# Kernel optimization log

Measured on AMD Instinct MI355X. Metric: run time of the kernel, lower is better.

The kernel has to match this reference:

```python
import jax, jax.numpy as jnp
import numpy as np

N = 50000      # nodes
E_BASE = 400000  # random edges (avg degree 8)
E = E_BASE + N   # + self loops (added by add_self_loops in the torch code)
D = 128        # in_channels == hidden_output


def gcn_conv(x, src, dst, w, W, b, n_nodes):
    """PyG GCNConv with precomputed self-loops: h = x@W + b; symmetric-norm scatter-add."""
    h = x @ W + b                                            # [N, H]
    deg = jax.ops.segment_sum(w, dst, num_segments=n_nodes)  # weighted in-degree
    dinv = jnp.where(deg > 0, jax.lax.rsqrt(deg), 0.0)
    norm = dinv[src] * w * dinv[dst]                         # [E]
    msg = h[src] * norm[:, None]                             # gather + scale
    return jax.ops.segment_sum(msg, dst, num_segments=n_nodes)


def prelu(z, alpha):
    return jnp.where(z >= 0, z, alpha[None, :] * z)


def gconv(x, src, dst, w, W1, b1, W2, b2, alpha, n_nodes):
    z = prelu(gcn_conv(x, src, dst, w, W1, b1, n_nodes), alpha)
    z = prelu(gcn_conv(z, src, dst, w, W2, b2, n_nodes), alpha)
    return z


def setup_inputs() -> dict:
    key = jax.random.key(0)
    ks = jax.random.split(key, 12)
    src = jax.random.randint(ks[0], (E_BASE,), 0, N)
    dst = jax.random.randint(ks[1], (E_BASE,), 0, N)
    loops = jnp.arange(N, dtype=src.dtype)
    edge_index = jnp.stack([jnp.concatenate([src, loops]),
                            jnp.concatenate([dst, loops])])
    # |time_encoder| output used as edge weight -> positive; self-loop fill_value=1.0
    edge_weight = jnp.concatenate([
        jax.random.uniform(ks[2], (E_BASE,), minval=0.1, maxval=1.0),
        jnp.ones((N,), jnp.float32)])
    x = jax.random.normal(ks[3], (N, D), jnp.float32)
    s = 1.0 / np.sqrt(D)
    def lin(k):
        return jax.random.uniform(k, (D, D), jnp.float32, -s, s)
    return {
        "x": x, "edge_index": edge_index, "edge_weight": edge_weight,
        "perm1": jax.random.permutation(ks[4], N),
        "perm2": jax.random.permutation(ks[5], N),
        "W1a": lin(ks[6]), "b1a": jnp.zeros((D,), jnp.float32),
        "W2a": lin(ks[7]), "b2a": jnp.zeros((D,), jnp.float32),
        "alpha1": jnp.full((D,), 0.25, jnp.float32),
        "W1b": lin(ks[8]), "b1b": jnp.zeros((D,), jnp.float32),
        "W2b": lin(ks[9]), "b2b": jnp.zeros((D,), jnp.float32),
        "alpha2": jnp.full((D,), 0.25, jnp.float32),
        "projW": lin(ks[10]), "projb": jnp.zeros((D,), jnp.float32),
    }


def reference(x, edge_index, edge_weight, perm1, perm2,
              W1a, b1a, W2a, b2a, alpha1,
              W1b, b1b, W2b, b2b, alpha2, projW, projb):
    src, dst = edge_index[0], edge_index[1]
    n = x.shape[0]
    # two views (Identity augmentors), two encoders
    z1 = gconv(x, src, dst, edge_weight, W1a, b1a, W2a, b2a, alpha1, n)
    z2 = gconv(x, src, dst, edge_weight, W1b, b1b, W2b, b2b, alpha2, n)
    g1 = jax.nn.sigmoid(z1.mean(axis=0, keepdims=True)) @ projW + projb  # [1, H]
    g2 = jax.nn.sigmoid(z2.mean(axis=0, keepdims=True)) @ projW + projb
    # corruption: permute node features, keep graph structure
    z1n = gconv(x[perm1], src, dst, edge_weight, W1a, b1a, W2a, b2a, alpha1, n)
    z2n = gconv(x[perm2], src, dst, edge_weight, W1b, b1b, W2b, b2b, alpha2, n)
    return (z1, z2, g1, g2, z1n, z2n)
```

## Files before the change

kernel.cpp:

```cpp
#include <hip/hip_runtime.h>
#include <math.h>

#define D 128

typedef __attribute__((ext_vector_type(8))) short bf16x8;
typedef __attribute__((ext_vector_type(4))) float f32x4;

__device__ __forceinline__ unsigned short f2bf(float f) {
  unsigned u = __float_as_uint(f);
  unsigned r = (u + 0x7fffu + ((u >> 16) & 1u)) >> 16;
  return (unsigned short)r;
}
__device__ __forceinline__ unsigned pack2bf(float x, float y) {
  return (unsigned)f2bf(x) | ((unsigned)f2bf(y) << 16);
}
__device__ __forceinline__ float bf_lo(unsigned u) { return __uint_as_float(u << 16); }
__device__ __forceinline__ float bf_hi(unsigned u) { return __uint_as_float(u & 0xffff0000u); }


__global__ __launch_bounds__(256) void hist_k(const int* __restrict__ dst,
    const float* __restrict__ w, float* __restrict__ deg,
    int* __restrict__ cnt, int E) {
  int e = blockIdx.x * 256 + threadIdx.x;
  if (e < E) {
    int d = dst[e];
    atomicAdd(&deg[d], w[e]);
    atomicAdd(&cnt[d], 1);
  }
}

__global__ __launch_bounds__(256) void scan1_k(const int* __restrict__ cnt,
    int* __restrict__ offs, int* __restrict__ bsum, int n) {
  __shared__ int ls[256];
  int t = threadIdx.x;
  int base = blockIdx.x * 1024 + t * 4;
  int v0 = 0, v1 = 0, v2 = 0, v3 = 0;
  if (base + 0 < n) v0 = cnt[base + 0];
  if (base + 1 < n) v1 = cnt[base + 1];
  if (base + 2 < n) v2 = cnt[base + 2];
  if (base + 3 < n) v3 = cnt[base + 3];
  int s = v0 + v1 + v2 + v3;
  ls[t] = s;
  __syncthreads();
  for (int off = 1; off < 256; off <<= 1) {
    int x = 0;
    if (t >= off) x = ls[t - off];
    __syncthreads();
    if (t >= off) ls[t] += x;
    __syncthreads();
  }
  int run = (t > 0) ? ls[t - 1] : 0;
  if (base + 0 < n) offs[base + 0] = run; run += v0;
  if (base + 1 < n) offs[base + 1] = run; run += v1;
  if (base + 2 < n) offs[base + 2] = run; run += v2;
  if (base + 3 < n) offs[base + 3] = run;
  if (t == 255) bsum[blockIdx.x] = ls[255];
}

__global__ void scan2_k(int* bsum, int nb) {
  if (threadIdx.x == 0) {
    int run = 0;
    for (int i = 0; i < nb; ++i) { int v = bsum[i]; bsum[i] = run; run += v; }
  }
}

__global__ __launch_bounds__(256) void scan3_k(int* __restrict__ offs,
    const int* __restrict__ bsum, int n, int total) {
  int t = threadIdx.x;
  int add = bsum[blockIdx.x];
  int base = blockIdx.x * 1024 + t * 4;
#pragma unroll
  for (int i = 0; i < 4; ++i)
    if (base + i < n) offs[base + i] += add;
  if (blockIdx.x == 0 && t == 0) offs[n] = total;
}

__global__ __launch_bounds__(256) void fillnorm_k(const int* __restrict__ src,
    const int* __restrict__ dst, const float* __restrict__ w,
    const float* __restrict__ deg, const int* __restrict__ perm1,
    const int* __restrict__ perm2, const int* __restrict__ offs,
    int* __restrict__ cur, int2* __restrict__ ep, int2* __restrict__ pp, int E) {
  int e = blockIdx.x * 256 + threadIdx.x;
  if (e >= E) return;
  int s = src[e], d = dst[e];
  float ds = deg[s], dd = deg[d];
  float a = ds > 0.f ? rsqrtf(ds) : 0.f;
  float b = dd > 0.f ? rsqrtf(dd) : 0.f;
  float nr = a * w[e] * b;
  int p = atomicAdd(&cur[d], 1);
  int pos = offs[d] + p;
  ep[pos] = make_int2(s, __float_as_int(nr));
  pp[pos] = make_int2(perm1[s], perm2[s]);
}


__global__ __launch_bounds__(256) void prep_k(const float* __restrict__ x,
    const float* __restrict__ W1a, const float* __restrict__ W2a,
    const float* __restrict__ W1b, const float* __restrict__ W2b,
    unsigned short* __restrict__ xb,
    unsigned short* __restrict__ F1a, unsigned short* __restrict__ F2a,
    unsigned short* __restrict__ F1b, unsigned short* __restrict__ F2b, int n) {
  int b = blockIdx.x, t = threadIdx.x;
  if (b < 32) {
    const float* Wsrc = (b < 8) ? W1a : (b < 16) ? W2a : (b < 24) ? W1b : W2b;
    unsigned short* Fdst = (b < 8) ? F1a : (b < 16) ? F2a : (b < 24) ? F1b : F2b;
    int u = ((b & 7) << 8) + t;
    int l = u & 63;
    int ct = (u >> 6) & 7;
    int kk5 = u >> 9;
    int nn = (ct << 4) + (l & 15);
    int kb = (kk5 << 5) + ((l >> 4) << 3);
    unsigned r0 = pack2bf(Wsrc[(kb + 0) * D + nn], Wsrc[(kb + 1) * D + nn]);
    unsigned r1 = pack2bf(Wsrc[(kb + 2) * D + nn], Wsrc[(kb + 3) * D + nn]);
    unsigned r2 = pack2bf(Wsrc[(kb + 4) * D + nn], Wsrc[(kb + 5) * D + nn]);
    unsigned r3 = pack2bf(Wsrc[(kb + 6) * D + nn], Wsrc[(kb + 7) * D + nn]);
    ((uint4*)Fdst)[u] = make_uint4(r0, r1, r2, r3);
  } else {
    size_t i = (size_t)(b - 32) * 256 + t;
    size_t total = (size_t)n * (D / 8);
    if (i < total) {
      const float4* xs = (const float4*)x;
      float4 a = xs[i * 2], c = xs[i * 2 + 1];
      ((uint4*)xb)[i] = make_uint4(pack2bf(a.x, a.y), pack2bf(a.z, a.w),
                                   pack2bf(c.x, c.y), pack2bf(c.z, c.w));
    }
  }
}


struct GemmArgs {
  const unsigned short* A[4];
  const unsigned short* W[4];
  const float* bias[4];
  unsigned short* out[4];
};

__global__ __launch_bounds__(256) void gemm_k(GemmArgs ga, int n) {
  int y = blockIdx.y;
  const unsigned short* A = ga.A[y];
  const unsigned short* Wf = ga.W[y];
  const float* bias = ga.bias[y];
  unsigned short* outb = ga.out[y];

  __shared__ __attribute__((aligned(16))) unsigned short Wl[16384];
  int t = threadIdx.x;
  {
    const uint4* srcp = (const uint4*)Wf;
    uint4* dstp = (uint4*)Wl;
#pragma unroll
    for (int i = 0; i < 8; ++i) dstp[t + (i << 8)] = srcp[t + (i << 8)];
  }
  __syncthreads();
  int wave = t >> 6, lane = t & 63;
  int row0 = (blockIdx.x << 6) + (wave << 4);
  int r = row0 + (lane & 15);
  int kg = (lane >> 4) << 3;
  f32x4 acc[8];
#pragma unroll
  for (int ct = 0; ct < 8; ++ct) {
    float bv = bias[(ct << 4) + (lane & 15)];
    acc[ct] = (f32x4){bv, bv, bv, bv};
  }
  bool inb = (r < n);
  const bf16x8* Wlv = (const bf16x8*)Wl;
#pragma unroll
  for (int ks = 0; ks < 4; ++ks) {
    bf16x8 a = {0, 0, 0, 0, 0, 0, 0, 0};
    if (inb) a = *(const bf16x8*)(A + (size_t)r * D + (ks << 5) + kg);
#pragma unroll
    for (int ct = 0; ct < 8; ++ct) {
      bf16x8 bb = Wlv[((ks << 3) + ct) * 64 + lane];
      acc[ct] = __builtin_amdgcn_mfma_f32_16x16x32_bf16(a, bb, acc[ct], 0, 0, 0);
    }
  }
  int orow = row0 + ((lane >> 4) << 2);
#pragma unroll
  for (int ct = 0; ct < 8; ++ct) {
    int col = (ct << 4) + (lane & 15);
#pragma unroll
    for (int v = 0; v < 4; ++v) {
      int rr = orow + v;
      if (rr < n) outb[(size_t)rr * D + col] = f2bf(acc[ct][v]);
    }
  }
}


__global__ __launch_bounds__(256) void aggL1_k(
    const unsigned* __restrict__ H0, const unsigned* __restrict__ H1,
    const int2* __restrict__ ep, const int2* __restrict__ pp,
    const int* __restrict__ offs,
    const float* __restrict__ al1, const float* __restrict__ al2,
    unsigned* __restrict__ oA0, unsigned* __restrict__ oP0,
    unsigned* __restrict__ oA1, unsigned* __restrict__ oP1, int n) {
  int y = blockIdx.y;
  const unsigned* Hb = y ? H1 : H0;
  const float* alpha = y ? al2 : al1;
  unsigned* OutA = y ? oA1 : oA0;
  unsigned* OutP = y ? oP1 : oP0;

  int wave = threadIdx.x >> 6, lane = threadIdx.x & 63;
  int node = blockIdx.x * 4 + wave;
  if (node >= n) return;
  int beg = offs[node], end = offs[node + 1];
  float2 a0 = make_float2(0.f, 0.f), a1 = make_float2(0.f, 0.f);
  int j = beg;
  for (; j + 2 <= end; j += 2) {
    int2 e0 = ep[j], e1 = ep[j + 1];
    int2 q0 = pp[j], q1 = pp[j + 1];
    float n0 = __int_as_float(e0.y), n1 = __int_as_float(e1.y);
    int p0 = y ? q0.y : q0.x;
    int p1 = y ? q1.y : q1.x;
    unsigned u0 = Hb[(size_t)e0.x * 64 + lane];
    unsigned u1 = Hb[(size_t)e1.x * 64 + lane];
    unsigned v0 = Hb[(size_t)p0 * 64 + lane];
    unsigned v1 = Hb[(size_t)p1 * 64 + lane];
    a0.x = fmaf(bf_lo(u0), n0, a0.x); a0.y = fmaf(bf_hi(u0), n0, a0.y);
    a0.x = fmaf(bf_lo(u1), n1, a0.x); a0.y = fmaf(bf_hi(u1), n1, a0.y);
    a1.x = fmaf(bf_lo(v0), n0, a1.x); a1.y = fmaf(bf_hi(v0), n0, a1.y);
    a1.x = fmaf(bf_lo(v1), n1, a1.x); a1.y = fmaf(bf_hi(v1), n1, a1.y);
  }
  if (j < end) {
    int2 e0 = ep[j];
    int2 q0 = pp[j];
    float n0 = __int_as_float(e0.y);
    int p0 = y ? q0.y : q0.x;
    unsigned u0 = Hb[(size_t)e0.x * 64 + lane];
    unsigned v0 = Hb[(size_t)p0 * 64 + lane];
    a0.x = fmaf(bf_lo(u0), n0, a0.x); a0.y = fmaf(bf_hi(u0), n0, a0.y);
    a1.x = fmaf(bf_lo(v0), n0, a1.x); a1.y = fmaf(bf_hi(v0), n0, a1.y);
  }
  float2 al = ((const float2*)alpha)[lane];
  float2 o0, o1;
  o0.x = a0.x >= 0.f ? a0.x : al.x * a0.x;
  o0.y = a0.y >= 0.f ? a0.y : al.y * a0.y;
  o1.x = a1.x >= 0.f ? a1.x : al.x * a1.x;
  o1.y = a1.y >= 0.f ? a1.y : al.y * a1.y;
  OutA[(size_t)node * 64 + lane] = pack2bf(o0.x, o0.y);
  OutP[(size_t)node * 64 + lane] = pack2bf(o1.x, o1.y);
}


__global__ __launch_bounds__(256) void aggF_k(
    const unsigned* __restrict__ I0, const unsigned* __restrict__ I1,
    const unsigned* __restrict__ I2, const unsigned* __restrict__ I3,
    const int2* __restrict__ ep, const int* __restrict__ offs,
    const float* __restrict__ al1, const float* __restrict__ al2,
    float* __restrict__ O0, float* __restrict__ O1,
    float* __restrict__ O2, float* __restrict__ O3,
    float* __restrict__ csum, int n) {
  int y = blockIdx.y;
  const unsigned* Hb = (y == 0) ? I0 : (y == 1) ? I1 : (y == 2) ? I2 : I3;
  float* Out = (y == 0) ? O0 : (y == 1) ? O1 : (y == 2) ? O2 : O3;
  const float* alpha = (y < 2) ? al1 : al2;
  int slot = (y == 0) ? 0 : (y == 2) ? 1 : -1;

  int wave = threadIdx.x >> 6, lane = threadIdx.x & 63;
  int node = blockIdx.x * 4 + wave;
  float2 o = make_float2(0.f, 0.f);
  if (node < n) {
    int beg = offs[node], end = offs[node + 1];
    float2 acc = make_float2(0.f, 0.f);
    int j = beg;
    for (; j + 4 <= end; j += 4) {
      int2 e0 = ep[j], e1 = ep[j + 1], e2 = ep[j + 2], e3 = ep[j + 3];
      unsigned u0 = Hb[(size_t)e0.x * 64 + lane];
      unsigned u1 = Hb[(size_t)e1.x * 64 + lane];
      unsigned u2 = Hb[(size_t)e2.x * 64 + lane];
      unsigned u3 = Hb[(size_t)e3.x * 64 + lane];
      float n0 = __int_as_float(e0.y), n1 = __int_as_float(e1.y);
      float n2 = __int_as_float(e2.y), n3 = __int_as_float(e3.y);
      acc.x = fmaf(bf_lo(u0), n0, acc.x); acc.y = fmaf(bf_hi(u0), n0, acc.y);
      acc.x = fmaf(bf_lo(u1), n1, acc.x); acc.y = fmaf(bf_hi(u1), n1, acc.y);
      acc.x = fmaf(bf_lo(u2), n2, acc.x); acc.y = fmaf(bf_hi(u2), n2, acc.y);
      acc.x = fmaf(bf_lo(u3), n3, acc.x); acc.y = fmaf(bf_hi(u3), n3, acc.y);
    }
    for (; j < end; ++j) {
      int2 e0 = ep[j];
      unsigned u0 = Hb[(size_t)e0.x * 64 + lane];
      float n0 = __int_as_float(e0.y);
      acc.x = fmaf(bf_lo(u0), n0, acc.x); acc.y = fmaf(bf_hi(u0), n0, acc.y);
    }
    float2 al = ((const float2*)alpha)[lane];
    o.x = acc.x >= 0.f ? acc.x : al.x * acc.x;
    o.y = acc.y >= 0.f ? acc.y : al.y * acc.y;
    ((float2*)(Out + (size_t)node * D))[lane] = o;
  }
  if (slot >= 0) {
    __shared__ float2 red[4][64];
    red[wave][lane] = o;
    __syncthreads();
    if (wave == 0) {
      float2 s0 = red[0][lane], s1 = red[1][lane];
      float2 s2 = red[2][lane], s3 = red[3][lane];
      float sx = s0.x + s1.x + s2.x + s3.x;
      float sy = s0.y + s1.y + s2.y + s3.y;
      float* base = csum + slot * 4096 + (blockIdx.x & 31) * 128;
      atomicAdd(&base[2 * lane], sx);
      atomicAdd(&base[2 * lane + 1], sy);
    }
  }
}


__global__ __launch_bounds__(128) void proj_k(const float* __restrict__ csum,
    const float* __restrict__ pW, const float* __restrict__ pb,
    float* __restrict__ g, float invN) {
  __shared__ float sg[128];
  int t = threadIdx.x;
  float s = 0.f;
#pragma unroll
  for (int i = 0; i < 32; ++i) s += csum[i * 128 + t];
  sg[t] = 1.f / (1.f + expf(-s * invN));
  __syncthreads();
  float a = pb[t];
  for (int k = 0; k < 128; ++k)
    a = fmaf(sg[k], pW[k * 128 + t], a);
  g[t] = a;
}


extern "C" void kernel_launch(void* const* d_in, const int* in_sizes, int n_in,
                              void* d_out, int out_size, void* d_ws, size_t ws_size,
                              hipStream_t stream) {
  const float* x   = (const float*)d_in[0];
  const int*   ei  = (const int*)d_in[1];
  const float* w   = (const float*)d_in[2];
  const int* perm1 = (const int*)d_in[3];
  const int* perm2 = (const int*)d_in[4];
  const float* W1a = (const float*)d_in[5];
  const float* b1a = (const float*)d_in[6];
  const float* W2a = (const float*)d_in[7];
  const float* b2a = (const float*)d_in[8];
  const float* al1 = (const float*)d_in[9];
  const float* W1b = (const float*)d_in[10];
  const float* b1b = (const float*)d_in[11];
  const float* W2b = (const float*)d_in[12];
  const float* b2b = (const float*)d_in[13];
  const float* al2 = (const float*)d_in[14];
  const float* pW  = (const float*)d_in[15];
  const float* pb  = (const float*)d_in[16];

  const int E = in_sizes[2];
  const int N = in_sizes[3];
  const int* srcA = ei;
  const int* dstA = ei + E;

  float* out = (float*)d_out;
  size_t ND = (size_t)N * D;
  float* z1  = out;
  float* z2  = out + ND;
  float* g1  = out + 2 * ND;
  float* g2  = g1 + D;
  float* z1n = g2 + D;
  float* z2n = z1n + ND;

  char* p = (char*)d_ws;
  auto carve = [&](size_t bytes) {
    char* r = p;
    p += (bytes + 255) & ~(size_t)255;
    return r;
  };
  float* deg  = (float*)carve((size_t)N * 4);
  int*   cnt  = (int*)carve((size_t)N * 4);
  int*   cur  = (int*)carve((size_t)N * 4);
  size_t zeroBytes = (size_t)((char*)(cur + N) - (char*)deg);
  int*   offs = (int*)carve((size_t)(N + 1) * 4);
  int*   bsum = (int*)carve(256 * 4);
  int2*  ep   = (int2*)carve((size_t)E * 8);
  int2*  pp   = (int2*)carve((size_t)E * 8);
  unsigned short* xb  = (unsigned short*)carve(ND * 2);
  unsigned short* h1a = (unsigned short*)carve(ND * 2);
  unsigned short* h1b = (unsigned short*)carve(ND * 2);
  unsigned short* yx  = (unsigned short*)carve(ND * 2);
  unsigned short* F1a = (unsigned short*)carve(32768);
  unsigned short* F2a = (unsigned short*)carve(32768);
  unsigned short* F1b = (unsigned short*)carve(32768);
  unsigned short* F2b = (unsigned short*)carve(32768);
  float* csum = (float*)carve(2 * 32 * 128 * 4);

  unsigned short* mAa = (unsigned short*)z1n;
  unsigned short* mPa = (unsigned short*)z1n + ND;
  unsigned short* mAb = (unsigned short*)z2n;
  unsigned short* mPb = (unsigned short*)z2n + ND;

  int nbE = (E + 255) / 256;
  int nbS = (N + 1023) / 1024;
  int nbA = (N + 3) / 4;
  int nbG = (N + 63) / 64;
  int nbP = 32 + (int)(((size_t)N * (D / 8) + 255) / 256);

  prep_k<<<nbP, 256, 0, stream>>>(x, W1a, W2a, W1b, W2b, xb, F1a, F2a, F1b, F2b, N);
  hipMemsetAsync(deg, 0, zeroBytes, stream);
  hipMemsetAsync(csum, 0, 2 * 32 * 128 * 4, stream);
  hist_k<<<nbE, 256, 0, stream>>>(dstA, w, deg, cnt, E);
  scan1_k<<<nbS, 256, 0, stream>>>(cnt, offs, bsum, N);
  scan2_k<<<1, 64, 0, stream>>>(bsum, nbS);
  scan3_k<<<nbS, 256, 0, stream>>>(offs, bsum, N, E);
  fillnorm_k<<<nbE, 256, 0, stream>>>(srcA, dstA, w, deg, perm1, perm2, offs,
                                      cur, ep, pp, E);

  GemmArgs g1a;
  g1a.A[0] = xb;  g1a.W[0] = F1a; g1a.bias[0] = b1a; g1a.out[0] = h1a;
  g1a.A[1] = xb;  g1a.W[1] = F1b; g1a.bias[1] = b1b; g1a.out[1] = h1b;
  g1a.A[2] = xb;  g1a.W[2] = F1a; g1a.bias[2] = b1a; g1a.out[2] = h1a;
  g1a.A[3] = xb;  g1a.W[3] = F1a; g1a.bias[3] = b1a; g1a.out[3] = h1a;
  gemm_k<<<dim3(nbG, 2), 256, 0, stream>>>(g1a, N);

  aggL1_k<<<dim3(nbA, 2), 256, 0, stream>>>(
      (const unsigned*)h1a, (const unsigned*)h1b, ep, pp, offs, al1, al2,
      (unsigned*)mAa, (unsigned*)mPa, (unsigned*)mAb, (unsigned*)mPb, N);

  GemmArgs g2a;
  g2a.A[0] = mAa; g2a.W[0] = F2a; g2a.bias[0] = b2a; g2a.out[0] = xb;
  g2a.A[1] = mPa; g2a.W[1] = F2a; g2a.bias[1] = b2a; g2a.out[1] = h1a;
  g2a.A[2] = mAb; g2a.W[2] = F2b; g2a.bias[2] = b2b; g2a.out[2] = h1b;
  g2a.A[3] = mPb; g2a.W[3] = F2b; g2a.bias[3] = b2b; g2a.out[3] = yx;
  gemm_k<<<dim3(nbG, 4), 256, 0, stream>>>(g2a, N);

  aggF_k<<<dim3(nbA, 4), 256, 0, stream>>>(
      (const unsigned*)xb, (const unsigned*)h1a, (const unsigned*)h1b,
      (const unsigned*)yx, ep, offs, al1, al2, z1, z1n, z2, z2n, csum, N);

  float invN = 1.0f / (float)N;
  proj_k<<<1, 128, 0, stream>>>(csum, pW, pb, g1, invN);
  proj_k<<<1, 128, 0, stream>>>(csum + 4096, pW, pb, g2, invN);
}
```

Measured before the change: 323.9 us.

## Merge per-stream aggregation grids into one four-stream aggregation kernel

Both aggregation kernels now handle all four feature streams (two encoders, clean and corrupted) per node in a single wave, instead of launching separate blockIdx.y slices per stream. The CSR offsets, edge indices and norms are loaded once and reused across the four gathers, and more independent loads are in flight per iteration. In exchange each wave uses more registers, which may lower occupancy, and the grid has a quarter (final layer) or half (first layer) as many blocks.

```diff
diff --git a/kernel.cpp b/kernel.cpp
--- a/kernel.cpp
+++ b/kernel.cpp
@@ -186,116 +186,103 @@
 }
 
 
-__global__ __launch_bounds__(256) void aggL1_k(
-    const unsigned* __restrict__ H0, const unsigned* __restrict__ H1,
+template <bool FINAL>
+__global__ __launch_bounds__(256) void agg4_k(
+    const unsigned* __restrict__ T0, const unsigned* __restrict__ T1,
+    const unsigned* __restrict__ T2, const unsigned* __restrict__ T3,
     const int2* __restrict__ ep, const int2* __restrict__ pp,
     const int* __restrict__ offs,
     const float* __restrict__ al1, const float* __restrict__ al2,
-    unsigned* __restrict__ oA0, unsigned* __restrict__ oP0,
-    unsigned* __restrict__ oA1, unsigned* __restrict__ oP1, int n) {
-  int y = blockIdx.y;
-  const unsigned* Hb = y ? H1 : H0;
-  const float* alpha = y ? al2 : al1;
-  unsigned* OutA = y ? oA1 : oA0;
-  unsigned* OutP = y ? oP1 : oP0;
-
+    unsigned* __restrict__ O0b, unsigned* __restrict__ O1b,
+    unsigned* __restrict__ O2b, unsigned* __restrict__ O3b,
+    float* __restrict__ O0f, float* __restrict__ O1f,
+    float* __restrict__ O2f, float* __restrict__ O3f,
+    float* __restrict__ csum, int n) {
   int wave = threadIdx.x >> 6, lane = threadIdx.x & 63;
   int node = blockIdx.x * 4 + wave;
-  if (node >= n) return;
-  int beg = offs[node], end = offs[node + 1];
   float2 a0 = make_float2(0.f, 0.f), a1 = make_float2(0.f, 0.f);
-  int j = beg;
-  for (; j + 2 <= end; j += 2) {
-    int2 e0 = ep[j], e1 = ep[j + 1];
-    int2 q0 = pp[j], q1 = pp[j + 1];
-    float n0 = __int_as_float(e0.y), n1 = __int_as_float(e1.y);
-    int p0 = y ? q0.y : q0.x;
-    int p1 = y ? q1.y : q1.x;
-    unsigned u0 = Hb[(size_t)e0.x * 64 + lane];
-    unsigned u1 = Hb[(size_t)e1.x * 64 + lane];
-    unsigned v0 = Hb[(size_t)p0 * 64 + lane];
-    unsigned v1 = Hb[(size_t)p1 * 64 + lane];
-    a0.x = fmaf(bf_lo(u0), n0, a0.x); a0.y = fmaf(bf_hi(u0), n0, a0.y);
-    a0.x = fmaf(bf_lo(u1), n1, a0.x); a0.y = fmaf(bf_hi(u1), n1, a0.y);
-    a1.x = fmaf(bf_lo(v0), n0, a1.x); a1.y = fmaf(bf_hi(v0), n0, a1.y);
-    a1.x = fmaf(bf_lo(v1), n1, a1.x); a1.y = fmaf(bf_hi(v1), n1, a1.y);
-  }
-  if (j < end) {
-    int2 e0 = ep[j];
-    int2 q0 = pp[j];
-    float n0 = __int_as_float(e0.y);
-    int p0 = y ? q0.y : q0.x;
-    unsigned u0 = Hb[(size_t)e0.x * 64 + lane];
-    unsigned v0 = Hb[(size_t)p0 * 64 + lane];
-    a0.x = fmaf(bf_lo(u0), n0, a0.x); a0.y = fmaf(bf_hi(u0), n0, a0.y);
-    a1.x = fmaf(bf_lo(v0), n0, a1.x); a1.y = fmaf(bf_hi(v0), n0, a1.y);
-  }
-  float2 al = ((const float2*)alpha)[lane];
-  float2 o0, o1;
-  o0.x = a0.x >= 0.f ? a0.x : al.x * a0.x;
-  o0.y = a0.y >= 0.f ? a0.y : al.y * a0.y;
-  o1.x = a1.x >= 0.f ? a1.x : al.x * a1.x;
-  o1.y = a1.y >= 0.f ? a1.y : al.y * a1.y;
-  OutA[(size_t)node * 64 + lane] = pack2bf(o0.x, o0.y);
-  OutP[(size_t)node * 64 + lane] = pack2bf(o1.x, o1.y);
-}
-
-
-__global__ __launch_bounds__(256) void aggF_k(
-    const unsigned* __restrict__ I0, const unsigned* __restrict__ I1,
-    const unsigned* __restrict__ I2, const unsigned* __restrict__ I3,
-    const int2* __restrict__ ep, const int* __restrict__ offs,
-    const float* __restrict__ al1, const float* __restrict__ al2,
-    float* __restrict__ O0, float* __restrict__ O1,
-    float* __restrict__ O2, float* __restrict__ O3,
-    float* __restrict__ csum, int n) {
-  int y = blockIdx.y;
-  const unsigned* Hb = (y == 0) ? I0 : (y == 1) ? I1 : (y == 2) ? I2 : I3;
-  float* Out = (y == 0) ? O0 : (y == 1) ? O1 : (y == 2) ? O2 : O3;
-  const float* alpha = (y < 2) ? al1 : al2;
-  int slot = (y == 0) ? 0 : (y == 2) ? 1 : -1;
-
-  int wave = threadIdx.x >> 6, lane = threadIdx.x & 63;
-  int node = blockIdx.x * 4 + wave;
-  float2 o = make_float2(0.f, 0.f);
+  float2 a2 = make_float2(0.f, 0.f), a3 = make_float2(0.f, 0.f);
+
   if (node < n) {
     int beg = offs[node], end = offs[node + 1];
-    float2 acc = make_float2(0.f, 0.f);
     int j = beg;
     for (; j + 4 <= end; j += 4) {
-      int2 e0 = ep[j], e1 = ep[j + 1], e2 = ep[j + 2], e3 = ep[j + 3];
-      unsigned u0 = Hb[(size_t)e0.x * 64 + lane];
-      unsigned u1 = Hb[(size_t)e1.x * 64 + lane];
-      unsigned u2 = Hb[(size_t)e2.x * 64 + lane];
-      unsigned u3 = Hb[(size_t)e3.x * 64 + lane];
-      float n0 = __int_as_float(e0.y), n1 = __int_as_float(e1.y);
-      float n2 = __int_as_float(e2.y), n3 = __int_as_float(e3.y);
-      acc.x = fmaf(bf_lo(u0), n0, acc.x); acc.y = fmaf(bf_hi(u0), n0, acc.y);
-      acc.x = fmaf(bf_lo(u1), n1, acc.x); acc.y = fmaf(bf_hi(u1), n1, acc.y);
-      acc.x = fmaf(bf_lo(u2), n2, acc.x); acc.y = fmaf(bf_hi(u2), n2, acc.y);
-      acc.x = fmaf(bf_lo(u3), n3, acc.x); acc.y = fmaf(bf_hi(u3), n3, acc.y);
+      unsigned g0[4], g1[4], g2[4], g3[4];
+      float nr[4];
+#pragma unroll
+      for (int u = 0; u < 4; ++u) {
+        int2 e = ep[j + u];
+        nr[u] = __int_as_float(e.y);
+        int s = e.x, ia = s, ib = s;
+        if constexpr (!FINAL) {
+          int2 q = pp[j + u];
+          ia = q.x; ib = q.y;
+        }
+        g0[u] = T0[(size_t)s * 64 + lane];
+        g1[u] = T1[(size_t)ia * 64 + lane];
+        g2[u] = T2[(size_t)s * 64 + lane];
+        g3[u] = T3[(size_t)ib * 64 + lane];
+      }
+#pragma unroll
+      for (int u = 0; u < 4; ++u) {
+        a0.x = fmaf(bf_lo(g0[u]), nr[u], a0.x); a0.y = fmaf(bf_hi(g0[u]), nr[u], a0.y);
+        a1.x = fmaf(bf_lo(g1[u]), nr[u], a1.x); a1.y = fmaf(bf_hi(g1[u]), nr[u], a1.y);
+        a2.x = fmaf(bf_lo(g2[u]), nr[u], a2.x); a2.y = fmaf(bf_hi(g2[u]), nr[u], a2.y);
+        a3.x = fmaf(bf_lo(g3[u]), nr[u], a3.x); a3.y = fmaf(bf_hi(g3[u]), nr[u], a3.y);
+      }
     }
     for (; j < end; ++j) {
-      int2 e0 = ep[j];
-      unsigned u0 = Hb[(size_t)e0.x * 64 + lane];
-      float n0 = __int_as_float(e0.y);
-      acc.x = fmaf(bf_lo(u0), n0, acc.x); acc.y = fmaf(bf_hi(u0), n0, acc.y);
-    }
-    float2 al = ((const float2*)alpha)[lane];
-    o.x = acc.x >= 0.f ? acc.x : al.x * acc.x;
-    o.y = acc.y >= 0.f ? acc.y : al.y * acc.y;
-    ((float2*)(Out + (size_t)node * D))[lane] = o;
-  }
-  if (slot >= 0) {
-    __shared__ float2 red[4][64];
-    red[wave][lane] = o;
+      int2 e = ep[j];
+      float nu = __int_as_float(e.y);
+      int s = e.x, ia = s, ib = s;
+      if constexpr (!FINAL) {
+        int2 q = pp[j];
+        ia = q.x; ib = q.y;
+      }
+      unsigned u0 = T0[(size_t)s * 64 + lane];
+      unsigned u1 = T1[(size_t)ia * 64 + lane];
+      unsigned u2 = T2[(size_t)s * 64 + lane];
+      unsigned u3 = T3[(size_t)ib * 64 + lane];
+      a0.x = fmaf(bf_lo(u0), nu, a0.x); a0.y = fmaf(bf_hi(u0), nu, a0.y);
+      a1.x = fmaf(bf_lo(u1), nu, a1.x); a1.y = fmaf(bf_hi(u1), nu, a1.y);
+      a2.x = fmaf(bf_lo(u2), nu, a2.x); a2.y = fmaf(bf_hi(u2), nu, a2.y);
+      a3.x = fmaf(bf_lo(u3), nu, a3.x); a3.y = fmaf(bf_hi(u3), nu, a3.y);
+    }
+  }
+
+  float2 alA = ((const float2*)al1)[lane];
+  float2 alB = ((const float2*)al2)[lane];
+  float2 o0 = make_float2(0.f, 0.f), o1 = o0, o2 = o0, o3 = o0;
+  if (node < n) {
+    o0.x = a0.x >= 0.f ? a0.x : alA.x * a0.x;  o0.y = a0.y >= 0.f ? a0.y : alA.y * a0.y;
+    o1.x = a1.x >= 0.f ? a1.x : alA.x * a1.x;  o1.y = a1.y >= 0.f ? a1.y : alA.y * a1.y;
+    o2.x = a2.x >= 0.f ? a2.x : alB.x * a2.x;  o2.y = a2.y >= 0.f ? a2.y : alB.y * a2.y;
+    o3.x = a3.x >= 0.f ? a3.x : alB.x * a3.x;  o3.y = a3.y >= 0.f ? a3.y : alB.y * a3.y;
+    size_t idx = (size_t)node * 64 + lane;
+    if constexpr (FINAL) {
+      ((float2*)O0f)[idx] = o0;
+      ((float2*)O1f)[idx] = o1;
+      ((float2*)O2f)[idx] = o2;
+      ((float2*)O3f)[idx] = o3;
+    } else {
+      O0b[idx] = pack2bf(o0.x, o0.y);
+      O1b[idx] = pack2bf(o1.x, o1.y);
+      O2b[idx] = pack2bf(o2.x, o2.y);
+      O3b[idx] = pack2bf(o3.x, o3.y);
+    }
+  }
+
+  if constexpr (FINAL) {
+    __shared__ float2 red[2][4][64];
+    red[0][wave][lane] = o0;
+    red[1][wave][lane] = o2;
     __syncthreads();
-    if (wave == 0) {
-      float2 s0 = red[0][lane], s1 = red[1][lane];
-      float2 s2 = red[2][lane], s3 = red[3][lane];
+    if (wave < 2) {
+      float2 s0 = red[wave][0][lane], s1 = red[wave][1][lane];
+      float2 s2 = red[wave][2][lane], s3 = red[wave][3][lane];
       float sx = s0.x + s1.x + s2.x + s3.x;
       float sy = s0.y + s1.y + s2.y + s3.y;
-      float* base = csum + slot * 4096 + (blockIdx.x & 31) * 128;
+      float* base = csum + wave * 4096 + (blockIdx.x & 31) * 128;
       atomicAdd(&base[2 * lane], sx);
       atomicAdd(&base[2 * lane + 1], sy);
     }
@@ -379,10 +366,10 @@
   unsigned short* F2b = (unsigned short*)carve(32768);
   float* csum = (float*)carve(2 * 32 * 128 * 4);
 
-  unsigned short* mAa = (unsigned short*)z1n;
-  unsigned short* mPa = (unsigned short*)z1n + ND;
-  unsigned short* mAb = (unsigned short*)z2n;
-  unsigned short* mPb = (unsigned short*)z2n + ND;
+  unsigned* mAa = (unsigned*)z1n;
+  unsigned* mPa = (unsigned*)z1n + ND / 2;
+  unsigned* mAb = (unsigned*)z2n;
+  unsigned* mPb = (unsigned*)z2n + ND / 2;
 
   int nbE = (E + 255) / 256;
   int nbS = (N + 1023) / 1024;
@@ -407,20 +394,26 @@
   g1a.A[3] = xb;  g1a.W[3] = F1a; g1a.bias[3] = b1a; g1a.out[3] = h1a;
   gemm_k<<<dim3(nbG, 2), 256, 0, stream>>>(g1a, N);
 
-  aggL1_k<<<dim3(nbA, 2), 256, 0, stream>>>(
-      (const unsigned*)h1a, (const unsigned*)h1b, ep, pp, offs, al1, al2,
-      (unsigned*)mAa, (unsigned*)mPa, (unsigned*)mAb, (unsigned*)mPb, N);
+  agg4_k<false><<<nbA, 256, 0, stream>>>(
+      (const unsigned*)h1a, (const unsigned*)h1a,
+      (const unsigned*)h1b, (const unsigned*)h1b,
+      ep, pp, offs, al1, al2,
+      mAa, mPa, mAb, mPb,
+      nullptr, nullptr, nullptr, nullptr, nullptr, N);
 
   GemmArgs g2a;
-  g2a.A[0] = mAa; g2a.W[0] = F2a; g2a.bias[0] = b2a; g2a.out[0] = xb;
-  g2a.A[1] = mPa; g2a.W[1] = F2a; g2a.bias[1] = b2a; g2a.out[1] = h1a;
-  g2a.A[2] = mAb; g2a.W[2] = F2b; g2a.bias[2] = b2b; g2a.out[2] = h1b;
-  g2a.A[3] = mPb; g2a.W[3] = F2b; g2a.bias[3] = b2b; g2a.out[3] = yx;
+  g2a.A[0] = (const unsigned short*)mAa; g2a.W[0] = F2a; g2a.bias[0] = b2a; g2a.out[0] = xb;
+  g2a.A[1] = (const unsigned short*)mPa; g2a.W[1] = F2a; g2a.bias[1] = b2a; g2a.out[1] = h1a;
+  g2a.A[2] = (const unsigned short*)mAb; g2a.W[2] = F2b; g2a.bias[2] = b2b; g2a.out[2] = h1b;
+  g2a.A[3] = (const unsigned short*)mPb; g2a.W[3] = F2b; g2a.bias[3] = b2b; g2a.out[3] = yx;
   gemm_k<<<dim3(nbG, 4), 256, 0, stream>>>(g2a, N);
 
-  aggF_k<<<dim3(nbA, 4), 256, 0, stream>>>(
-      (const unsigned*)xb, (const unsigned*)h1a, (const unsigned*)h1b,
-      (const unsigned*)yx, ep, offs, al1, al2, z1, z1n, z2, z2n, csum, N);
+  agg4_k<true><<<nbA, 256, 0, stream>>>(
+      (const unsigned*)xb, (const unsigned*)h1a,
+      (const unsigned*)h1b, (const unsigned*)yx,
+      ep, nullptr, offs, al1, al2,
+      nullptr, nullptr, nullptr, nullptr,
+      z1, z1n, z2, z2n, csum, N);
 
   float invN = 1.0f / (float)N;
   proj_k<<<1, 128, 0, stream>>>(csum, pW, pb, g1, invN);
```

Measured after the change: 288.0 us. 11.1% less time.
